# Kernel tuning notes

Hardware: AMD Instinct MI355X
Metric: run time of the kernel (lower is better)

## Reference

```python
import jax, jax.numpy as jnp
import numpy as np

B, T, DIM, H = 2, 2048, 1024, 16
DH = DIM // H  # head dim = 64, rope half = 32


def _apply_rope(q, k):
    # q,k: [b,h,t,d]
    b, h, t, d = q.shape
    half = d // 2
    idx = jnp.arange(half, dtype=jnp.float32)
    pos = jnp.arange(t, dtype=jnp.float32)[:, None]
    inv = 10000.0 ** (-2.0 * idx / (2.0 * half))
    ang = pos * inv  # [t, half]
    cos = jnp.cos(ang).astype(q.dtype)[None, None]  # [1,1,t,half]
    sin = jnp.sin(ang).astype(q.dtype)[None, None]

    def rot(x):
        a = x[..., :half]
        b2 = x[..., half:2 * half]
        return jnp.concatenate([a * cos - b2 * sin, a * sin + b2 * cos], axis=-1)

    return rot(q), rot(k)


def setup_inputs() -> dict:
    key = jax.random.key(0)
    k0, k1, k2 = jax.random.split(key, 3)
    x = jax.random.normal(k0, (B, T, DIM), dtype=jnp.float32)
    mask = jnp.tril(jnp.ones((T, T), dtype=jnp.int32))[None, None]  # causal [1,1,T,T]
    scale = DIM ** -0.5
    W_qkv = jax.random.normal(k1, (DIM, 3 * DIM), dtype=jnp.float32) * scale
    b_qkv = jnp.zeros((3 * DIM,), dtype=jnp.float32)
    W_out = jax.random.normal(k2, (DIM, DIM), dtype=jnp.float32) * scale
    b_out = jnp.zeros((DIM,), dtype=jnp.float32)
    return {"x": x, "mask": mask, "W_qkv": W_qkv, "b_qkv": b_qkv,
            "W_out": W_out, "b_out": b_out}


def reference(x, mask, W_qkv, b_qkv, W_out, b_out):
    b, t, c = x.shape
    qkv = x @ W_qkv + b_qkv  # [b,t,3c]
    q, k, v = jnp.split(qkv, 3, axis=-1)
    q = q.reshape(b, t, H, DH).transpose(0, 2, 1, 3)  # [b,h,t,dh]
    k = k.reshape(b, t, H, DH).transpose(0, 2, 1, 3)
    v = v.reshape(b, t, H, DH).transpose(0, 2, 1, 3)
    q, k = _apply_rope(q, k)
    s = jnp.einsum('bhqd,bhkd->bhqk', q, k) * (DH ** -0.5)
    s = jnp.where(mask == 0, -jnp.inf, s)
    p = jax.nn.softmax(s, axis=-1)  # dropout is identity (drop=0.0)
    y = jnp.einsum('bhqk,bhkd->bhqd', p, v)
    y = y.transpose(0, 2, 1, 3).reshape(b, t, c)
    return y @ W_out + b_out
```

## Files before the change

### kernel.cpp

```cpp
#include <hip/hip_runtime.h>
#include <hip/hip_bf16.h>
#include <math.h>

#define BB 2
#define TT 2048
#define DIMM 1024
#define HH 16
#define DHH 64

typedef _Float16 half8_t __attribute__((ext_vector_type(8)));
typedef _Float16 half4_t __attribute__((ext_vector_type(4)));
typedef float floatx4 __attribute__((ext_vector_type(4)));

typedef const unsigned int __attribute__((address_space(1)))* gp_t;
typedef unsigned int __attribute__((address_space(3)))* lp_t;

__device__ __forceinline__ void async16(const void* g, void* l) {
    __builtin_amdgcn_global_load_lds((gp_t)g, (lp_t)l, 16, 0, 0);
}

template <int CTRL>
__device__ __forceinline__ float dppmov(float x) {
    return __builtin_bit_cast(float, __builtin_amdgcn_update_dpp(
        0, __builtin_bit_cast(int, x), CTRL, 0xf, 0xf, false));
}
__device__ __forceinline__ float rowred_sum(float v) {
    v += dppmov<0x128>(v);
    v += dppmov<0x124>(v);
    v += dppmov<0x122>(v);
    v += dppmov<0x121>(v);
    return v;
}

__global__ void rope_table(float2* __restrict__ tab) {
    int idx = blockIdx.x * 256 + threadIdx.x;
    int t = idx >> 5, d = idx & 31;
    float inv = __expf(-(float)d * 0.28782313662425572f);
    float ang = (float)t * inv;
    float s, c;
    __sincosf(ang, &s, &c);
    tab[idx] = make_float2(c, s);
}

__global__ void convert_f32_to_f16(const float* __restrict__ x, _Float16* __restrict__ y, int n) {
    int i = (blockIdx.x * blockDim.x + threadIdx.x) * 4;
    floatx4 v = *(const floatx4*)(x + i);
    half4_t h;
    h[0] = (_Float16)v[0]; h[1] = (_Float16)v[1];
    h[2] = (_Float16)v[2]; h[3] = (_Float16)v[3];
    *(half4_t*)(y + i) = h;
}

__global__ void transpose_to_f16(const float* __restrict__ W, _Float16* __restrict__ Wt, int K, int N) {
    __shared__ float tile[32][33];
    int n0 = blockIdx.x * 32, k0 = blockIdx.y * 32;
    int tx = threadIdx.x, ty = threadIdx.y;
    for (int i = 0; i < 32; i += 8)
        tile[ty + i][tx] = W[(size_t)(k0 + ty + i) * N + n0 + tx];
    __syncthreads();
    for (int i = 0; i < 32; i += 8)
        Wt[(size_t)(n0 + ty + i) * K + k0 + tx] = (_Float16)tile[tx][ty + i];
}

template <int BN, int MODE>
__global__ __launch_bounds__(256) void gemm_ld_kernel(
    const _Float16* __restrict__ A, const _Float16* __restrict__ Bt,
    const float* __restrict__ bias, float* __restrict__ C,
    _Float16* __restrict__ Qr, _Float16* __restrict__ Kr, _Float16* __restrict__ Vt,
    const float2* __restrict__ tab,
    int M, int N, int K) {
    constexpr int NB = (BN == 128) ? 4 : 2;
    __shared__ __align__(16) _Float16 As[128 * 32];
    __shared__ __align__(16) _Float16 Bs[BN * 32];
    int tid = threadIdx.x;
    int m0 = blockIdx.y * 128, n0 = blockIdx.x * BN;
    int wave = tid >> 6, lane = tid & 63;
    int wm = (wave & 1) * 64;
    int wn = (wave >> 1) * (BN / 2);
    int lm = lane & 15, quad = lane >> 4;

    floatx4 acc[4][NB] = {};

    int srow = tid >> 2;
    int scol = (tid & 3) * 8;

    for (int k0 = 0; k0 < K; k0 += 32) {
        {
            const _Float16* g0 = A + (size_t)(m0 + srow) * K + k0 + scol;
            async16(g0, (char*)As + (wave * 64) * 16);
            const _Float16* g1 = A + (size_t)(m0 + 64 + srow) * K + k0 + scol;
            async16(g1, (char*)As + (256 + wave * 64) * 16);
        }
        {
            const _Float16* g0 = Bt + (size_t)(n0 + srow) * K + k0 + scol;
            async16(g0, (char*)Bs + (wave * 64) * 16);
            if (BN == 128) {
                const _Float16* g1 = Bt + (size_t)(n0 + 64 + srow) * K + k0 + scol;
                async16(g1, (char*)Bs + (256 + wave * 64) * 16);
            }
        }
        __syncthreads();

        half8_t af[4], bf[NB];
        for (int mb = 0; mb < 4; mb++)
            af[mb] = *(const half8_t*)&As[(wm + mb * 16 + lm) * 32 + quad * 8];
        for (int nb = 0; nb < NB; nb++)
            bf[nb] = *(const half8_t*)&Bs[(wn + nb * 16 + lm) * 32 + quad * 8];
        for (int mb = 0; mb < 4; mb++)
            for (int nb = 0; nb < NB; nb++)
                acc[mb][nb] = __builtin_amdgcn_mfma_f32_16x16x32_f16(af[mb], bf[nb], acc[mb][nb], 0, 0, 0);
        __syncthreads();
    }

    if (MODE == 0) {
        for (int mb = 0; mb < 4; mb++) {
            int row = m0 + wm + mb * 16 + quad * 4;
            for (int nb = 0; nb < NB; nb++) {
                int col = n0 + wn + nb * 16 + lm;
                float bv = bias[col];
                for (int r = 0; r < 4; r++)
                    C[(size_t)(row + r) * N + col] = acc[mb][nb][r] + bv;
            }
        }
    } else {
        int col0 = n0 + wn;
        int sect = col0 >> 10;
        int h = (col0 & 1023) >> 6;
        if (sect < 2) {
            _Float16* dst = (sect == 0) ? Qr : Kr;
            float fscale = (sect == 0) ? 0.18033688011112042f : 1.0f;
            for (int nb = 0; nb < 2; nb++) {
                int d = nb * 16 + lm;
                float bva = bias[col0 + d];
                float bvb = bias[col0 + d + 32];
                for (int mb = 0; mb < 4; mb++) {
                    int row = m0 + wm + mb * 16 + quad * 4;
                    int b = row >> 11;
                    size_t ob0 = ((size_t)(b * HH + h) * TT) * 64;
                    for (int r = 0; r < 4; r++) {
                        int t = (row + r) & 2047;
                        float2 cs = tab[t * 32 + d];
                        float va = acc[mb][nb][r] + bva;
                        float vb = acc[mb][nb + 2][r] + bvb;
                        size_t ob = ob0 + (size_t)t * 64;
                        dst[ob + d] = (_Float16)((va * cs.x - vb * cs.y) * fscale);
                        dst[ob + d + 32] = (_Float16)((va * cs.y + vb * cs.x) * fscale);
                    }
                }
            }
        } else {
            for (int nb = 0; nb < 4; nb++) {
                int d = nb * 16 + lm;
                float bv = bias[col0 + d];
                for (int mb = 0; mb < 4; mb++) {
                    int row = m0 + wm + mb * 16 + quad * 4;
                    int b = row >> 11;
                    int t = row & 2047;
                    half4_t pv;
                    for (int r = 0; r < 4; r++) pv[r] = (_Float16)(acc[mb][nb][r] + bv);
                    *(half4_t*)&Vt[((size_t)(b * HH + h) * 64 + d) * TT + t] = pv;
                }
            }
        }
    }
}

__device__ const unsigned char kBlkMap[24] = {
    30, 28, 26, 24, 22, 20, 18, 16, 14, 31,
    12, 29, 10, 27, 8, 25, 6, 23, 4, 21, 2, 19, 0, 17};

__global__ __launch_bounds__(256, 3) void flash_attn(
    const _Float16* __restrict__ Qr, const _Float16* __restrict__ Kr,
    const _Float16* __restrict__ Vt,
    _Float16* __restrict__ Po, float* __restrict__ Pls) {
    int bh = blockIdx.y;
    int code = kBlkMap[blockIdx.x];
    int iq = code >> 1, ic = code & 1;
    int kstart = ic * 16;
    int kend = min(kstart + 16, 2 * iq + 2);

    int tid = threadIdx.x, wave = tid >> 6, lane = tid & 63;
    int lm = lane & 15, quad = lane >> 4;
    int q0w = iq * 128 + wave * 32;

    __shared__ __align__(16) _Float16 Ks[2][64 * 64];
    __shared__ __align__(16) _Float16 Vs[2][64 * 64];
    __shared__ __align__(16) _Float16 Pbuf[4][32 * 64];
    _Float16* plds = Pbuf[wave];

    const _Float16* Qbase = Qr + ((size_t)bh * TT + q0w) * 64;
    half8_t aq[2][2];
    for (int mb = 0; mb < 2; mb++) {
        aq[mb][0] = *(const half8_t*)(Qbase + (size_t)(mb * 16 + lm) * 64 + quad * 8);
        aq[mb][1] = *(const half8_t*)(Qbase + (size_t)(mb * 16 + lm) * 64 + 32 + quad * 8);
    }

    const _Float16* Kb = Kr + (size_t)bh * TT * 64;
    const _Float16* Vb = Vt + (size_t)bh * 64 * TT;

    floatx4 o[2][4] = {};
    float lsum[2][4] = {};

    auto stage = [&](int kt, int buf) {
        int k0 = kt * 64;
        for (int i = 0; i < 2; i++) {
            int sl = i * 256 + tid;
            int row = sl >> 3;
            int c = (sl & 7) ^ (row & 7);
            async16(Kb + (size_t)(k0 + row) * 64 + c * 8, (char*)&Ks[buf][0] + sl * 16);
            async16(Vb + (size_t)row * TT + k0 + c * 8, (char*)&Vs[buf][0] + sl * 16);
        }
    };

    stage(kstart, 0);

    for (int kt = kstart; kt < kend; ++kt) {
        int buf = (kt - kstart) & 1;
        __syncthreads();
        if (kt + 1 < kend) stage(kt + 1, buf ^ 1);
        int k0 = kt * 64;
        if (k0 > q0w + 31) continue;

        floatx4 s4[2][4] = {};
        for (int nb = 0; nb < 4; nb++) {
            int row = nb * 16 + lm, sw = row & 7;
            half8_t kb0 = *(const half8_t*)&Ks[buf][row * 64 + ((quad ^ sw) << 3)];
            half8_t kb1 = *(const half8_t*)&Ks[buf][row * 64 + (((4 + quad) ^ sw) << 3)];
            for (int mb = 0; mb < 2; mb++) {
                s4[mb][nb] = __builtin_amdgcn_mfma_f32_16x16x32_f16(aq[mb][0], kb0, s4[mb][nb], 0, 0, 0);
                s4[mb][nb] = __builtin_amdgcn_mfma_f32_16x16x32_f16(aq[mb][1], kb1, s4[mb][nb], 0, 0, 0);
            }
        }

        if (k0 + 63 > q0w) {
            for (int mb = 0; mb < 2; mb++)
                for (int nb = 0; nb < 4; nb++) {
                    int col = k0 + nb * 16 + lm;
                    int rowq = q0w + mb * 16 + quad * 4;
                    for (int r = 0; r < 4; r++)
                        if (col > rowq + r) s4[mb][nb][r] = -1e30f;
                }
        }

        for (int mb = 0; mb < 2; mb++)
            for (int nb = 0; nb < 4; nb++) {
                int cbase = nb * 2 + (lm >> 3);
                for (int r = 0; r < 4; r++) {
                    float p = __builtin_amdgcn_exp2f(s4[mb][nb][r]);
                    lsum[mb][r] += p;
                    int prow = mb * 16 + quad * 4 + r;
                    plds[prow * 64 + ((cbase ^ (prow & 7)) << 3) + (lm & 7)] = (_Float16)p;
                }
            }
        asm volatile("s_waitcnt lgkmcnt(0)" ::: "memory");
        int psw = lm & 7;
        half8_t pa[2][2];
        for (int mp = 0; mp < 2; mp++) {
            pa[mp][0] = *(const half8_t*)&plds[(mp * 16 + lm) * 64 + ((quad ^ psw) << 3)];
            pa[mp][1] = *(const half8_t*)&plds[(mp * 16 + lm) * 64 + (((4 + quad) ^ psw) << 3)];
        }
        asm volatile("" ::: "memory");

        for (int db = 0; db < 4; db++) {
            int row = db * 16 + lm, sw = row & 7;
            half8_t vb0 = *(const half8_t*)&Vs[buf][row * 64 + ((quad ^ sw) << 3)];
            half8_t vb1 = *(const half8_t*)&Vs[buf][row * 64 + (((4 + quad) ^ sw) << 3)];
            for (int mb = 0; mb < 2; mb++) {
                o[mb][db] = __builtin_amdgcn_mfma_f32_16x16x32_f16(pa[mb][0], vb0, o[mb][db], 0, 0, 0);
                o[mb][db] = __builtin_amdgcn_mfma_f32_16x16x32_f16(pa[mb][1], vb1, o[mb][db], 0, 0, 0);
            }
        }
    }

    float lred[2][4];
    for (int mb = 0; mb < 2; mb++)
        for (int r = 0; r < 4; r++)
            lred[mb][r] = rowred_sum(lsum[mb][r]);

    size_t pbase = ((size_t)(bh * 16 + iq) * 2 + ic) * 8192;
    for (int mb = 0; mb < 2; mb++)
        for (int db = 0; db < 4; db++)
            for (int r = 0; r < 4; r++) {
                int row = wave * 32 + mb * 16 + quad * 4 + r;
                Po[pbase + row * 64 + db * 16 + lm] = (_Float16)o[mb][db][r];
            }
    if (lm == 0) {
        size_t lb = ((size_t)(bh * 16 + iq) * 2 + ic) * 128;
        for (int mb = 0; mb < 2; mb++)
            for (int r = 0; r < 4; r++)
                Pls[lb + wave * 32 + mb * 16 + quad * 4 + r] = lred[mb][r];
    }
}

__global__ __launch_bounds__(256) void attn_combine(
    const _Float16* __restrict__ Po, const float* __restrict__ Pls,
    _Float16* __restrict__ Yb) {
    int iq = blockIdx.x, bh = blockIdx.y;
    int b = bh >> 4, h = bh & 15;
    int tid = threadIdx.x;
    int row = tid >> 1, cg = (tid & 1) * 32;

    size_t base = ((size_t)(bh * 16 + iq) * 2) * 8192 + row * 64 + cg;
    size_t lb = ((size_t)(bh * 16 + iq) * 2) * 128 + row;
    float l = Pls[lb];
    float acc[32];
    {
        const half8_t* p = (const half8_t*)&Po[base];
        for (int j = 0; j < 4; j++) {
            half8_t v = p[j];
            for (int i = 0; i < 8; i++) acc[j * 8 + i] = (float)v[i];
        }
    }
    if (iq >= 8) {
        l += Pls[lb + 128];
        const half8_t* p = (const half8_t*)&Po[base + 8192];
        for (int j = 0; j < 4; j++) {
            half8_t v = p[j];
            for (int i = 0; i < 8; i++) acc[j * 8 + i] += (float)v[i];
        }
    }
    float inv = 1.0f / l;
    size_t yb = ((size_t)(b * TT) + iq * 128 + row) * DIMM + h * 64 + cg;
    for (int j = 0; j < 4; j++) {
        half8_t v;
        for (int i = 0; i < 8; i++) v[i] = (_Float16)(acc[j * 8 + i] * inv);
        *(half8_t*)&Yb[yb + j * 8] = v;
    }
}

extern "C" void kernel_launch(void* const* d_in, const int* in_sizes, int n_in,
                              void* d_out, int out_size, void* d_ws, size_t ws_size,
                              hipStream_t stream) {
    const float* x = (const float*)d_in[0];
    const float* W_qkv = (const float*)d_in[2];
    const float* b_qkv = (const float*)d_in[3];
    const float* W_out = (const float*)d_in[4];
    const float* b_out = (const float*)d_in[5];
    float* out = (float*)d_out;

    char* ws = (char*)d_ws;
    _Float16* xb = (_Float16*)ws;   ws += (size_t)4096 * 1024 * 2;
    _Float16* Wqt = (_Float16*)ws;  ws += (size_t)3072 * 1024 * 2;
    _Float16* Wot = (_Float16*)ws;  ws += (size_t)1024 * 1024 * 2;
    _Float16* Qr = (_Float16*)ws;   ws += (size_t)32 * 2048 * 64 * 2;
    _Float16* Kr = (_Float16*)ws;   ws += (size_t)32 * 2048 * 64 * 2;
    _Float16* Vt = (_Float16*)ws;   ws += (size_t)32 * 2048 * 64 * 2;
    _Float16* Yb = (_Float16*)ws;   ws += (size_t)4096 * 1024 * 2;
    float2* tab = (float2*)ws;      ws += (size_t)2048 * 32 * 8;
    _Float16* Po = (_Float16*)ws;   ws += (size_t)32 * 16 * 2 * 8192 * 2;
    float* Pls = (float*)ws;        ws += (size_t)32 * 16 * 2 * 128 * 4;

    rope_table<<<256, 256, 0, stream>>>(tab);
    convert_f32_to_f16<<<4096, 256, 0, stream>>>(x, xb, 4096 * 1024);
    transpose_to_f16<<<dim3(96, 32), dim3(32, 8), 0, stream>>>(W_qkv, Wqt, 1024, 3072);
    transpose_to_f16<<<dim3(32, 32), dim3(32, 8), 0, stream>>>(W_out, Wot, 1024, 1024);

    gemm_ld_kernel<128, 1><<<dim3(24, 32), 256, 0, stream>>>(
        xb, Wqt, b_qkv, nullptr, Qr, Kr, Vt, tab, 4096, 3072, 1024);

    flash_attn<<<dim3(24, 32), 256, 0, stream>>>(Qr, Kr, Vt, Po, Pls);
    attn_combine<<<dim3(16, 32), 256, 0, stream>>>(Po, Pls, Yb);

    gemm_ld_kernel<64, 0><<<dim3(16, 32), 256, 0, stream>>>(
        Yb, Wot, b_out, out, nullptr, nullptr, nullptr, nullptr, 4096, 1024, 1024);
}
```

Before: 218.2 us.

## Merge prep kernels into one launch and double-buffer GEMM LDS tiles

Replaces the four preprocessing launches (rope table, x conversion, two weight transposes) with a single prep_kernel that dispatches on block index, which removes per-launch overhead. The GEMM kernel now double-buffers its A and B shared-memory tiles so the async load of the next K slice overlaps the MFMA work on the current one, and it needs one barrier per iteration instead of two. This doubles LDS use per block, which may lower occupancy. It also relies on the single barrier to cover both the completion of the async global-to-LDS loads and the reuse of each buffer.

```diff
diff --git a/kernel.cpp b/kernel.cpp
--- a/kernel.cpp
+++ b/kernel.cpp
@@ -32,34 +32,45 @@
     return v;
 }
 
-__global__ void rope_table(float2* __restrict__ tab) {
-    int idx = blockIdx.x * 256 + threadIdx.x;
-    int t = idx >> 5, d = idx & 31;
-    float inv = __expf(-(float)d * 0.28782313662425572f);
-    float ang = (float)t * inv;
-    float s, c;
-    __sincosf(ang, &s, &c);
-    tab[idx] = make_float2(c, s);
-}
-
-__global__ void convert_f32_to_f16(const float* __restrict__ x, _Float16* __restrict__ y, int n) {
-    int i = (blockIdx.x * blockDim.x + threadIdx.x) * 4;
-    floatx4 v = *(const floatx4*)(x + i);
-    half4_t h;
-    h[0] = (_Float16)v[0]; h[1] = (_Float16)v[1];
-    h[2] = (_Float16)v[2]; h[3] = (_Float16)v[3];
-    *(half4_t*)(y + i) = h;
-}
-
-__global__ void transpose_to_f16(const float* __restrict__ W, _Float16* __restrict__ Wt, int K, int N) {
+__global__ __launch_bounds__(256) void prep_kernel(
+    const float* __restrict__ x, _Float16* __restrict__ xb,
+    const float* __restrict__ W_qkv, _Float16* __restrict__ Wqt,
+    const float* __restrict__ W_out, _Float16* __restrict__ Wot,
+    float2* __restrict__ tab) {
     __shared__ float tile[32][33];
-    int n0 = blockIdx.x * 32, k0 = blockIdx.y * 32;
-    int tx = threadIdx.x, ty = threadIdx.y;
-    for (int i = 0; i < 32; i += 8)
-        tile[ty + i][tx] = W[(size_t)(k0 + ty + i) * N + n0 + tx];
-    __syncthreads();
-    for (int i = 0; i < 32; i += 8)
-        Wt[(size_t)(n0 + ty + i) * K + k0 + tx] = (_Float16)tile[tx][ty + i];
+    int bid = blockIdx.x, tid = threadIdx.x;
+    if (bid < 4096) {
+        int i = (bid * 256 + tid) * 4;
+        floatx4 v = *(const floatx4*)(x + i);
+        half4_t h;
+        h[0] = (_Float16)v[0]; h[1] = (_Float16)v[1];
+        h[2] = (_Float16)v[2]; h[3] = (_Float16)v[3];
+        *(half4_t*)(xb + i) = h;
+    } else if (bid < 8192) {
+        const float* W; _Float16* Wt; int K, N, bx, by;
+        if (bid < 7168) {
+            W = W_qkv; Wt = Wqt; K = 1024; N = 3072;
+            int b2 = bid - 4096; bx = b2 % 96; by = b2 / 96;
+        } else {
+            W = W_out; Wt = Wot; K = 1024; N = 1024;
+            int b2 = bid - 7168; bx = b2 & 31; by = b2 >> 5;
+        }
+        int n0 = bx * 32, k0 = by * 32;
+        int tx = tid & 31, ty = tid >> 5;
+        for (int i = 0; i < 32; i += 8)
+            tile[ty + i][tx] = W[(size_t)(k0 + ty + i) * N + n0 + tx];
+        __syncthreads();
+        for (int i = 0; i < 32; i += 8)
+            Wt[(size_t)(n0 + ty + i) * K + k0 + tx] = (_Float16)tile[tx][ty + i];
+    } else {
+        int idx = (bid - 8192) * 256 + tid;
+        int t = idx >> 5, d = idx & 31;
+        float inv = __expf(-(float)d * 0.28782313662425572f);
+        float ang = (float)t * inv;
+        float s, c;
+        __sincosf(ang, &s, &c);
+        tab[idx] = make_float2(c, s);
+    }
 }
 
 template <int BN, int MODE>
@@ -70,8 +81,8 @@
     const float2* __restrict__ tab,
     int M, int N, int K) {
     constexpr int NB = (BN == 128) ? 4 : 2;
-    __shared__ __align__(16) _Float16 As[128 * 32];
-    __shared__ __align__(16) _Float16 Bs[BN * 32];
+    __shared__ __align__(16) _Float16 As[2][128 * 32];
+    __shared__ __align__(16) _Float16 Bs[2][BN * 32];
     int tid = threadIdx.x;
     int m0 = blockIdx.y * 128, n0 = blockIdx.x * BN;
     int wave = tid >> 6, lane = tid & 63;
@@ -84,32 +95,34 @@
     int srow = tid >> 2;
     int scol = (tid & 3) * 8;
 
-    for (int k0 = 0; k0 < K; k0 += 32) {
-        {
-            const _Float16* g0 = A + (size_t)(m0 + srow) * K + k0 + scol;
-            async16(g0, (char*)As + (wave * 64) * 16);
-            const _Float16* g1 = A + (size_t)(m0 + 64 + srow) * K + k0 + scol;
-            async16(g1, (char*)As + (256 + wave * 64) * 16);
-        }
-        {
-            const _Float16* g0 = Bt + (size_t)(n0 + srow) * K + k0 + scol;
-            async16(g0, (char*)Bs + (wave * 64) * 16);
-            if (BN == 128) {
-                const _Float16* g1 = Bt + (size_t)(n0 + 64 + srow) * K + k0 + scol;
-                async16(g1, (char*)Bs + (256 + wave * 64) * 16);
-            }
-        }
+    auto stage = [&](int k0, int buf) {
+        const _Float16* g0 = A + (size_t)(m0 + srow) * K + k0 + scol;
+        async16(g0, (char*)&As[buf][0] + (wave * 64) * 16);
+        const _Float16* g1 = A + (size_t)(m0 + 64 + srow) * K + k0 + scol;
+        async16(g1, (char*)&As[buf][0] + (256 + wave * 64) * 16);
+        const _Float16* gb0 = Bt + (size_t)(n0 + srow) * K + k0 + scol;
+        async16(gb0, (char*)&Bs[buf][0] + (wave * 64) * 16);
+        if (BN == 128) {
+            const _Float16* gb1 = Bt + (size_t)(n0 + 64 + srow) * K + k0 + scol;
+            async16(gb1, (char*)&Bs[buf][0] + (256 + wave * 64) * 16);
+        }
+    };
+
+    int nIt = K >> 5;
+    stage(0, 0);
+    for (int it = 0; it < nIt; ++it) {
+        int buf = it & 1;
         __syncthreads();
+        if (it + 1 < nIt) stage((it + 1) << 5, buf ^ 1);
 
         half8_t af[4], bf[NB];
         for (int mb = 0; mb < 4; mb++)
-            af[mb] = *(const half8_t*)&As[(wm + mb * 16 + lm) * 32 + quad * 8];
+            af[mb] = *(const half8_t*)&As[buf][(wm + mb * 16 + lm) * 32 + quad * 8];
         for (int nb = 0; nb < NB; nb++)
-            bf[nb] = *(const half8_t*)&Bs[(wn + nb * 16 + lm) * 32 + quad * 8];
+            bf[nb] = *(const half8_t*)&Bs[buf][(wn + nb * 16 + lm) * 32 + quad * 8];
         for (int mb = 0; mb < 4; mb++)
             for (int nb = 0; nb < NB; nb++)
                 acc[mb][nb] = __builtin_amdgcn_mfma_f32_16x16x32_f16(af[mb], bf[nb], acc[mb][nb], 0, 0, 0);
-        __syncthreads();
     }
 
     if (MODE == 0) {
@@ -350,10 +363,7 @@
     _Float16* Po = (_Float16*)ws;   ws += (size_t)32 * 16 * 2 * 8192 * 2;
     float* Pls = (float*)ws;        ws += (size_t)32 * 16 * 2 * 128 * 4;
 
-    rope_table<<<256, 256, 0, stream>>>(tab);
-    convert_f32_to_f16<<<4096, 256, 0, stream>>>(x, xb, 4096 * 1024);
-    transpose_to_f16<<<dim3(96, 32), dim3(32, 8), 0, stream>>>(W_qkv, Wqt, 1024, 3072);
-    transpose_to_f16<<<dim3(32, 32), dim3(32, 8), 0, stream>>>(W_out, Wot, 1024, 1024);
+    prep_kernel<<<8448, 256, 0, stream>>>(x, xb, W_qkv, Wqt, W_out, Wot, tab);
 
     gemm_ld_kernel<128, 1><<<dim3(24, 32), 256, 0, stream>>>(
         xb, Wqt, b_qkv, nullptr, Qr, Kr, Vt, tab, 4096, 3072, 1024);
```

New measurement: 205.9 us. 5.6% less time.
